# Optimization experiments

Hardware: AMD Instinct MI355X
Metric: run time of the kernel (lower is better)

## Reference

```python
import jax, jax.numpy as jnp
import numpy as np

P = 50000      # number of graph nodes (cortical dipoles)
HID = 256      # hidden width
E = 800000     # number of nonzeros in Ahat (avg degree 16)


def setup_inputs() -> dict:
    key = jax.random.key(0)
    ks = jax.random.split(key, 12)
    beta = jax.random.normal(ks[0], (P, 1), dtype=jnp.float32)
    degree = jax.random.uniform(ks[1], (P, 1), dtype=jnp.float32)
    A_rows = jax.random.randint(ks[2], (E,), 0, P, dtype=jnp.int32)
    A_cols = jax.random.randint(ks[3], (E,), 0, P, dtype=jnp.int32)
    # normalized-adjacency-like positive values
    A_vals = jax.random.uniform(ks[4], (E,), dtype=jnp.float32) * (1.0 / 16.0)
    # parameters (torch nn.Linear stores weight as [out, in])
    s_in = 1.0 / np.sqrt(3.0)
    s_h = 1.0 / np.sqrt(HID)
    W_in = jax.random.uniform(ks[5], (HID, 3), jnp.float32, -s_in, s_in)
    b_in = jax.random.uniform(ks[6], (HID,), jnp.float32, -s_in, s_in)
    W_mp1 = jax.random.uniform(ks[7], (HID, HID), jnp.float32, -s_h, s_h)
    W_mp2 = jax.random.uniform(ks[8], (HID, HID), jnp.float32, -s_h, s_h)
    W_out = jax.random.uniform(ks[9], (1, HID), jnp.float32, -s_h, s_h)
    b_out = jax.random.uniform(ks[10], (1,), jnp.float32, -s_h, s_h)
    return {
        "beta": beta, "degree": degree,
        "A_rows": A_rows, "A_cols": A_cols, "A_vals": A_vals,
        "W_in": W_in, "b_in": b_in,
        "W_mp1": W_mp1, "W_mp2": W_mp2,
        "W_out": W_out, "b_out": b_out,
    }


def _spmm(A_rows, A_cols, A_vals, X):
    # sparse [P,P] @ dense [P,H] via gather + segment-sum over COO edges
    msgs = A_vals[:, None] * X[A_cols]            # [E, H]
    return jax.ops.segment_sum(msgs, A_rows, num_segments=P)


def reference(beta, degree, A_rows, A_cols, A_vals,
              W_in, b_in, W_mp1, W_mp2, W_out, b_out):
    x = jnp.concatenate([beta, beta ** 2, degree], axis=1)   # [P, 3]
    h = jax.nn.relu(x @ W_in.T + b_in)                       # [P, HID]
    AH = _spmm(A_rows, A_cols, A_vals, h)                    # one-hop
    A2H = _spmm(A_rows, A_cols, A_vals, AH)                  # two-hop
    h = jax.nn.relu(AH @ W_mp1.T + A2H @ W_mp2.T)            # fused sum + relu
    g = jax.nn.softplus(h @ W_out.T + b_out)                 # [P, 1]
    return g
```

## Files before the change

kernel.cpp:

```cpp
#include <hip/hip_runtime.h>
#include <math.h>

#define NP 50000
#define HIDDEN 256
#define NE 800000
#define CAP 64

#define NSLICE 8
#define SLICE_ROWS 6250
#define BPS 256

#define OFF_AH     0ULL
#define OFF_A2H    25600000ULL
#define OFF_BP     51200000ULL
#define OFF_CNT    51462144ULL
#define OFF_PC     51662144ULL
#define OFF_EV     52062144ULL

typedef __attribute__((ext_vector_type(8))) short bf16x8;
typedef __attribute__((ext_vector_type(8))) unsigned short u16x8;
typedef __attribute__((ext_vector_type(4))) float f32x4;

__device__ inline unsigned short f2bf(float f) {
    union { float f; unsigned int u; } x; x.f = f;
    unsigned int r = x.u + 0x7FFFu + ((x.u >> 16) & 1u);
    return (unsigned short)(r >> 16);
}
__device__ inline float bf2f(unsigned short u) {
    union { unsigned int u; float f; } x; x.u = ((unsigned int)u) << 16; return x.f;
}

__global__ void bp_kernel(const float* __restrict__ W1,
                          const float* __restrict__ W2,
                          unsigned short* __restrict__ Bp) {
    int t = blockIdx.x * 256 + threadIdx.x;
    int j = t >> 9;
    int k = t & 511;
    float v = (k < 256) ? W1[j * 256 + k] : W2[j * 256 + (k - 256)];
    Bp[(k >> 3) * 2048 + j * 8 + (k & 7)] = f2bf(v);
}

__global__ void pc_kernel(const float* __restrict__ beta,
                          const float* __restrict__ degree,
                          float2* __restrict__ pc) {
    int i = blockIdx.x * 256 + threadIdx.x;
    if (i < NP) pc[i] = make_float2(beta[i], degree[i]);
}

__global__ __launch_bounds__(256) void scatter_sliced(
        const int* __restrict__ rows, const int* __restrict__ cols,
        const float* __restrict__ vals,
        int* __restrict__ cnt, int2* __restrict__ ev) {
    int slice = blockIdx.x & (NSLICE - 1);
    int bj = blockIdx.x >> 3;
    int rlo = slice * SLICE_ROWS;
    int rhi = rlo + SLICE_ROWS;
    for (int e = bj * 256 + threadIdx.x; e < NE; e += BPS * 256) {
        int r = rows[e];
        if (r >= rlo && r < rhi) {
            int pos = atomicAdd(&cnt[r], 1);
            if (pos < CAP)
                ev[(size_t)r * CAP + pos] = make_int2(cols[e], __float_as_int(vals[e]));
        }
    }
}

__global__ __launch_bounds__(256) void spmm_embed_kernel(
        const int* __restrict__ cnt, const int2* __restrict__ ev,
        const float2* __restrict__ pc,
        const float* __restrict__ W_in, const float* __restrict__ b_in,
        unsigned short* __restrict__ Y) {
    int w = threadIdx.x >> 6;
    int lane = threadIdx.x & 63;
    int r = blockIdx.x * 4 + w;
    if (r >= NP) return;
    int half = lane >> 5;
    int fo = (lane & 31) * 8;

    int n = min(cnt[r], CAP);
    int2 e2 = make_int2(0, 0);
    if (lane < n) e2 = ev[(size_t)r * CAP + lane];
    int col_l = e2.x;
    float val_l = __int_as_float(e2.y);

    float wr0[8], wr1[8], wr2[8], br[8];
    #pragma unroll
    for (int j = 0; j < 8; ++j) {
        wr0[j] = W_in[(fo + j) * 3 + 0];
        wr1[j] = W_in[(fo + j) * 3 + 1];
        wr2[j] = W_in[(fo + j) * 3 + 2];
        br[j]  = b_in[fo + j];
    }

    float acc[8] = {0.f,0.f,0.f,0.f,0.f,0.f,0.f,0.f};

#define ESTEP(d)                                                             \
    {                                                                        \
        float2 pr[d]; float vr[d];                                           \
        _Pragma("unroll")                                                    \
        for (int k = 0; k < (d); ++k) {                                      \
            int e = i + 2 * k + half;                                        \
            int c = __shfl(col_l, e);                                        \
            vr[k] = __shfl(val_l, e);                                        \
            pr[k] = pc[c];                                                   \
        }                                                                    \
        _Pragma("unroll")                                                    \
        for (int k = 0; k < (d); ++k) {                                      \
            float b = pr[k].x, dd = pr[k].y, v = vr[k];                      \
            float b2 = b * b;                                                \
            _Pragma("unroll")                                                \
            for (int j = 0; j < 8; ++j) {                                    \
                float t = fmaf(b, wr0[j], fmaf(b2, wr1[j], fmaf(dd, wr2[j], br[j]))); \
                acc[j] = fmaf(v, fmaxf(t, 0.f), acc[j]);                     \
            }                                                                \
        }                                                                    \
    }

    int i = 0;
    for (; i + 16 <= n; i += 16) ESTEP(8)
    if (i + 8 <= n) { ESTEP(4) i += 8; }
    if (i + 4 <= n) { ESTEP(2) i += 4; }
    if (i < n)      { ESTEP(2) }
#undef ESTEP

    #pragma unroll
    for (int j = 0; j < 8; ++j) acc[j] += __shfl_xor(acc[j], 32);
    if (half == 0) {
        u16x8 o;
        #pragma unroll
        for (int j = 0; j < 8; ++j) o[j] = f2bf(acc[j]);
        *reinterpret_cast<u16x8*>(Y + (size_t)r * HIDDEN + fo) = o;
    }
}

__global__ __launch_bounds__(256) void spmm_gather_kernel(
        const int* __restrict__ cnt, const int2* __restrict__ ev,
        const unsigned short* __restrict__ X,
        unsigned short* __restrict__ Y) {
    int w = threadIdx.x >> 6;
    int lane = threadIdx.x & 63;
    int r = blockIdx.x * 4 + w;
    if (r >= NP) return;
    int half = lane >> 5;
    int fo = (lane & 31) * 8;

    int n = min(cnt[r], CAP);
    int2 e2 = make_int2(0, 0);
    if (lane < n) e2 = ev[(size_t)r * CAP + lane];
    int col_l = e2.x;
    float val_l = __int_as_float(e2.y);

    float acc[8] = {0.f,0.f,0.f,0.f,0.f,0.f,0.f,0.f};

#define GSTEP(d)                                                             \
    {                                                                        \
        u16x8 xr[d]; float vr[d];                                            \
        _Pragma("unroll")                                                    \
        for (int k = 0; k < (d); ++k) {                                      \
            int e = i + 2 * k + half;                                        \
            int c = __shfl(col_l, e);                                        \
            vr[k] = __shfl(val_l, e);                                        \
            xr[k] = *reinterpret_cast<const u16x8*>(X + (size_t)c * HIDDEN + fo); \
        }                                                                    \
        _Pragma("unroll")                                                    \
        for (int k = 0; k < (d); ++k)                                        \
            _Pragma("unroll")                                                \
            for (int j = 0; j < 8; ++j)                                      \
                acc[j] = fmaf(vr[k], bf2f(xr[k][j]), acc[j]);                \
    }

    int i = 0;
    for (; i + 16 <= n; i += 16) GSTEP(8)
    if (i + 8 <= n) { GSTEP(4) i += 8; }
    if (i + 4 <= n) { GSTEP(2) i += 4; }
    if (i < n)      { GSTEP(2) }
#undef GSTEP

    #pragma unroll
    for (int j = 0; j < 8; ++j) acc[j] += __shfl_xor(acc[j], 32);
    if (half == 0) {
        u16x8 o;
        #pragma unroll
        for (int j = 0; j < 8; ++j) o[j] = f2bf(acc[j]);
        *reinterpret_cast<u16x8*>(Y + (size_t)r * HIDDEN + fo) = o;
    }
}

__global__ __launch_bounds__(512, 4) void mp_out_kernel(
        const unsigned short* __restrict__ AH,
        const unsigned short* __restrict__ A2H,
        const unsigned short* __restrict__ Bp,
        const float* __restrict__ W_out, const float* __restrict__ b_out,
        float* __restrict__ g) {
    __shared__ unsigned short As[128 * 64];
    __shared__ unsigned short Bs[8 * 256 * 8];
    __shared__ float Ps[4][128];

    int tid = threadIdx.x;
    int w = tid >> 6;
    int lane = tid & 63;
    int wr = w >> 2;
    int wc = w & 3;
    int p0 = blockIdx.x * 128;

    f32x4 acc[4][4];
    #pragma unroll
    for (int i = 0; i < 4; ++i)
        #pragma unroll
        for (int j = 0; j < 4; ++j)
            acc[i][j] = (f32x4){0.f, 0.f, 0.f, 0.f};

    for (int kc = 0; kc < 8; ++kc) {
        const unsigned short* Xsrc = (kc < 4) ? AH : A2H;
        int k0 = (kc & 3) * 64;
        __syncthreads();
        #pragma unroll
        for (int it = 0; it < 2; ++it) {
            int slot = it * 512 + tid;
            int ss = slot ^ ((slot >> 3) & 7);
            int row = ss >> 3;
            int ko = (ss & 7) * 8;
            int grow = p0 + row;
            if (grow >= NP) grow = NP - 1;
            float4 v = *reinterpret_cast<const float4*>(Xsrc + (size_t)grow * HIDDEN + k0 + ko);
            *reinterpret_cast<float4*>(&As[slot * 8]) = v;
        }
        #pragma unroll
        for (int it = 0; it < 4; ++it) {
            int c2 = it * 512 + tid;
            float4 v = *reinterpret_cast<const float4*>(
                Bp + ((size_t)(kc * 8 + (c2 >> 8))) * 2048 + (c2 & 255) * 8);
            *reinterpret_cast<float4*>(&Bs[c2 * 8]) = v;
        }
        __syncthreads();
        #pragma unroll
        for (int ks = 0; ks < 2; ++ks) {
            bf16x8 af[4], bfr[4];
            #pragma unroll
            for (int rt = 0; rt < 4; ++rt) {
                int row = wr * 64 + rt * 16 + (lane & 15);
                int elem = row * 64 + ks * 32 + (lane >> 4) * 8;
                elem ^= (row & 7) << 3;
                af[rt] = *reinterpret_cast<const bf16x8*>(&As[elem]);
            }
            #pragma unroll
            for (int nt = 0; nt < 4; ++nt) {
                int col = wc * 64 + nt * 16 + (lane & 15);
                int kbl = ks * 4 + (lane >> 4);
                bfr[nt] = *reinterpret_cast<const bf16x8*>(&Bs[kbl * 2048 + col * 8]);
            }
            #pragma unroll
            for (int rt = 0; rt < 4; ++rt)
                #pragma unroll
                for (int nt = 0; nt < 4; ++nt)
                    acc[rt][nt] = __builtin_amdgcn_mfma_f32_16x16x32_bf16(
                        af[rt], bfr[nt], acc[rt][nt], 0, 0, 0);
        }
    }

    float wv[4];
    #pragma unroll
    for (int nt = 0; nt < 4; ++nt)
        wv[nt] = W_out[wc * 64 + nt * 16 + (lane & 15)];

    float ps[4][4];
    #pragma unroll
    for (int rt = 0; rt < 4; ++rt)
        #pragma unroll
        for (int r = 0; r < 4; ++r) {
            float s = 0.f;
            #pragma unroll
            for (int nt = 0; nt < 4; ++nt)
                s = fmaf(fmaxf(acc[rt][nt][r], 0.0f), wv[nt], s);
            ps[rt][r] = s;
        }
    #pragma unroll
    for (int m = 1; m < 16; m <<= 1)
        #pragma unroll
        for (int rt = 0; rt < 4; ++rt)
            #pragma unroll
            for (int r = 0; r < 4; ++r)
                ps[rt][r] += __shfl_xor(ps[rt][r], m);

    if ((lane & 15) == 0) {
        int rb = wr * 64 + (lane >> 4) * 4;
        #pragma unroll
        for (int rt = 0; rt < 4; ++rt)
            #pragma unroll
            for (int r = 0; r < 4; ++r)
                Ps[wc][rb + rt * 16 + r] = ps[rt][r];
    }
    __syncthreads();
    if (tid < 128) {
        int p = p0 + tid;
        if (p < NP) {
            float z = Ps[0][tid] + Ps[1][tid] + Ps[2][tid] + Ps[3][tid] + b_out[0];
            g[p] = fmaxf(z, 0.0f) + log1pf(expf(-fabsf(z)));
        }
    }
}

extern "C" void kernel_launch(void* const* d_in, const int* in_sizes, int n_in,
                              void* d_out, int out_size, void* d_ws, size_t ws_size,
                              hipStream_t stream) {
    const float* beta   = (const float*)d_in[0];
    const float* degree = (const float*)d_in[1];
    const int*   A_rows = (const int*)d_in[2];
    const int*   A_cols = (const int*)d_in[3];
    const float* A_vals = (const float*)d_in[4];
    const float* W_in   = (const float*)d_in[5];
    const float* b_in   = (const float*)d_in[6];
    const float* W_mp1  = (const float*)d_in[7];
    const float* W_mp2  = (const float*)d_in[8];
    const float* W_out  = (const float*)d_in[9];
    const float* b_out  = (const float*)d_in[10];
    float* g = (float*)d_out;

    char* ws = (char*)d_ws;
    unsigned short* AH  = (unsigned short*)(ws + OFF_AH);
    unsigned short* A2H = (unsigned short*)(ws + OFF_A2H);
    unsigned short* Bp  = (unsigned short*)(ws + OFF_BP);
    int*    cnt = (int*)(ws + OFF_CNT);
    float2* pc  = (float2*)(ws + OFF_PC);
    int2*   ev  = (int2*)(ws + OFF_EV);

    hipMemsetAsync(cnt, 0, NP * sizeof(int), stream);

    bp_kernel<<<512, 256, 0, stream>>>(W_mp1, W_mp2, Bp);
    pc_kernel<<<(NP + 255) / 256, 256, 0, stream>>>(beta, degree, pc);

    scatter_sliced<<<NSLICE * BPS, 256, 0, stream>>>(A_rows, A_cols, A_vals, cnt, ev);

    spmm_embed_kernel<<<(NP + 3) / 4, 256, 0, stream>>>(cnt, ev, pc, W_in, b_in, AH);
    spmm_gather_kernel<<<(NP + 3) / 4, 256, 0, stream>>>(cnt, ev, AH, A2H);

    mp_out_kernel<<<(NP + 127) / 128, 512, 0, stream>>>(AH, A2H, Bp, W_out, b_out, g);
}
```

Measured before the change: 171.1 us.

## Merge prep kernels, vectorize scatter loads, direct-to-LDS tile loads, fix tail steps

Folds the memset, weight repack and pc packing into one prep kernel to cut launch count. The scatter kernel now reads row indices four at a time with int4 loads. The GEMM tile staging switches to global_load_lds so data goes straight into shared memory without passing through registers. The SpMM tail steps now mask out-of-range edges explicitly instead of reusing the generic step macro. Together these aim to cut launch overhead and memory-instruction cost, with some risk to correctness of the LDS layout and swizzle.

```diff
diff --git a/kernel.cpp b/kernel.cpp
--- a/kernel.cpp
+++ b/kernel.cpp
@@ -30,21 +30,33 @@
     union { unsigned int u; float f; } x; x.u = ((unsigned int)u) << 16; return x.f;
 }
 
-__global__ void bp_kernel(const float* __restrict__ W1,
-                          const float* __restrict__ W2,
-                          unsigned short* __restrict__ Bp) {
-    int t = blockIdx.x * 256 + threadIdx.x;
-    int j = t >> 9;
-    int k = t & 511;
-    float v = (k < 256) ? W1[j * 256 + k] : W2[j * 256 + (k - 256)];
-    Bp[(k >> 3) * 2048 + j * 8 + (k & 7)] = f2bf(v);
-}
-
-__global__ void pc_kernel(const float* __restrict__ beta,
-                          const float* __restrict__ degree,
-                          float2* __restrict__ pc) {
-    int i = blockIdx.x * 256 + threadIdx.x;
-    if (i < NP) pc[i] = make_float2(beta[i], degree[i]);
+__device__ __forceinline__ void gload16(const void* g, void* l) {
+    __builtin_amdgcn_global_load_lds(
+        (const __attribute__((address_space(1))) unsigned int*)g,
+        (__attribute__((address_space(3))) unsigned int*)l, 16, 0, 0);
+}
+
+__global__ void prep_kernel(const float* __restrict__ W1,
+                            const float* __restrict__ W2,
+                            unsigned short* __restrict__ Bp,
+                            const float* __restrict__ beta,
+                            const float* __restrict__ degree,
+                            float2* __restrict__ pc,
+                            int* __restrict__ cnt) {
+    int b = blockIdx.x;
+    if (b < 512) {
+        int t = b * 256 + threadIdx.x;
+        int j = t >> 9;
+        int k = t & 511;
+        float v = (k < 256) ? W1[j * 256 + k] : W2[j * 256 + (k - 256)];
+        Bp[(k >> 3) * 2048 + j * 8 + (k & 7)] = f2bf(v);
+    } else if (b < 708) {
+        int i = (b - 512) * 256 + threadIdx.x;
+        if (i < NP) pc[i] = make_float2(beta[i], degree[i]);
+    } else {
+        int i = (b - 708) * 256 + threadIdx.x;
+        if (i < NP) cnt[i] = 0;
+    }
 }
 
 __global__ __launch_bounds__(256) void scatter_sliced(
@@ -55,12 +67,17 @@
     int bj = blockIdx.x >> 3;
     int rlo = slice * SLICE_ROWS;
     int rhi = rlo + SLICE_ROWS;
-    for (int e = bj * 256 + threadIdx.x; e < NE; e += BPS * 256) {
-        int r = rows[e];
-        if (r >= rlo && r < rhi) {
-            int pos = atomicAdd(&cnt[r], 1);
-            if (pos < CAP)
-                ev[(size_t)r * CAP + pos] = make_int2(cols[e], __float_as_int(vals[e]));
+    for (int e0 = (bj * 256 + threadIdx.x) * 4; e0 < NE; e0 += BPS * 256 * 4) {
+        int4 r4 = *reinterpret_cast<const int4*>(rows + e0);
+        #pragma unroll
+        for (int q = 0; q < 4; ++q) {
+            int r = (q == 0) ? r4.x : (q == 1) ? r4.y : (q == 2) ? r4.z : r4.w;
+            if (r >= rlo && r < rhi) {
+                int e = e0 + q;
+                int pos = atomicAdd(&cnt[r], 1);
+                if (pos < CAP)
+                    ev[(size_t)r * CAP + pos] = make_int2(cols[e], __float_as_int(vals[e]));
+            }
         }
     }
 }
@@ -120,7 +137,28 @@
     for (; i + 16 <= n; i += 16) ESTEP(8)
     if (i + 8 <= n) { ESTEP(4) i += 8; }
     if (i + 4 <= n) { ESTEP(2) i += 4; }
-    if (i < n)      { ESTEP(2) }
+    if (i < n) {
+        float2 pr[2]; float vr[2];
+        #pragma unroll
+        for (int k = 0; k < 2; ++k) {
+            int e = i + 2 * k + half;
+            int es = (e < n) ? e : 0;
+            int c = __shfl(col_l, es);
+            float vt = __shfl(val_l, es);
+            vr[k] = (e < n) ? vt : 0.f;
+            pr[k] = pc[c];
+        }
+        #pragma unroll
+        for (int k = 0; k < 2; ++k) {
+            float b = pr[k].x, dd = pr[k].y, v = vr[k];
+            float b2 = b * b;
+            #pragma unroll
+            for (int j = 0; j < 8; ++j) {
+                float t = fmaf(b, wr0[j], fmaf(b2, wr1[j], fmaf(dd, wr2[j], br[j])));
+                acc[j] = fmaf(v, fmaxf(t, 0.f), acc[j]);
+            }
+        }
+    }
 #undef ESTEP
 
     #pragma unroll
@@ -173,7 +211,23 @@
     for (; i + 16 <= n; i += 16) GSTEP(8)
     if (i + 8 <= n) { GSTEP(4) i += 8; }
     if (i + 4 <= n) { GSTEP(2) i += 4; }
-    if (i < n)      { GSTEP(2) }
+    if (i < n) {
+        u16x8 xr[2]; float vr[2];
+        #pragma unroll
+        for (int k = 0; k < 2; ++k) {
+            int e = i + 2 * k + half;
+            int es = (e < n) ? e : 0;
+            int c = __shfl(col_l, es);
+            float vt = __shfl(val_l, es);
+            vr[k] = (e < n) ? vt : 0.f;
+            xr[k] = *reinterpret_cast<const u16x8*>(X + (size_t)c * HIDDEN + fo);
+        }
+        #pragma unroll
+        for (int k = 0; k < 2; ++k)
+            #pragma unroll
+            for (int j = 0; j < 8; ++j)
+                acc[j] = fmaf(vr[k], bf2f(xr[k][j]), acc[j]);
+    }
 #undef GSTEP
 
     #pragma unroll
@@ -222,15 +276,14 @@
             int ko = (ss & 7) * 8;
             int grow = p0 + row;
             if (grow >= NP) grow = NP - 1;
-            float4 v = *reinterpret_cast<const float4*>(Xsrc + (size_t)grow * HIDDEN + k0 + ko);
-            *reinterpret_cast<float4*>(&As[slot * 8]) = v;
+            gload16(Xsrc + (size_t)grow * HIDDEN + k0 + ko,
+                    &As[(size_t)(it * 512 + w * 64) * 8]);
         }
         #pragma unroll
         for (int it = 0; it < 4; ++it) {
             int c2 = it * 512 + tid;
-            float4 v = *reinterpret_cast<const float4*>(
-                Bp + ((size_t)(kc * 8 + (c2 >> 8))) * 2048 + (c2 & 255) * 8);
-            *reinterpret_cast<float4*>(&Bs[c2 * 8]) = v;
+            gload16(Bp + ((size_t)(kc * 8 + (c2 >> 8))) * 2048 + (c2 & 255) * 8,
+                    &Bs[(size_t)(it * 512 + w * 64) * 8]);
         }
         __syncthreads();
         #pragma unroll
@@ -324,10 +377,7 @@
     float2* pc  = (float2*)(ws + OFF_PC);
     int2*   ev  = (int2*)(ws + OFF_EV);
 
-    hipMemsetAsync(cnt, 0, NP * sizeof(int), stream);
-
-    bp_kernel<<<512, 256, 0, stream>>>(W_mp1, W_mp2, Bp);
-    pc_kernel<<<(NP + 255) / 256, 256, 0, stream>>>(beta, degree, pc);
+    prep_kernel<<<904, 256, 0, stream>>>(W_mp1, W_mp2, Bp, beta, degree, pc, cnt);
 
     scatter_sliced<<<NSLICE * BPS, 256, 0, stream>>>(A_rows, A_cols, A_vals, cnt, ev);
 
```

After: 161.5 us (median of 2 runs). -5.6%, faster.
